# Kernel optimization log

Measured on AMD Instinct MI355X. Metric: run time of the kernel, lower is better.

## Reference

```python
import jax, jax.numpy as jnp
import numpy as np

B, K, N = 32768, 8, 64
TN = 3 * N


def _P():
    # 9x9 vec-transpose permutation (matches the hand-built P in the torch module)
    P = np.zeros((9, 9), dtype=np.float32)
    rows = [0, 1, 2, 3, 4, 5, 6, 7, 8]
    cols = [0, 3, 6, 1, 4, 7, 2, 5, 8]
    P[rows, cols] = 1.0
    return jnp.asarray(P)


def _precompute(b, w, lam):
    # b: (K,3,N), w: (1,N,1), lam: scalar
    wsum = jnp.sum(w)
    b_w = (b @ w)[..., 0] / wsum                       # (K,3)
    sw = jnp.sqrt(w).reshape(1, 1, N)                  # (1,1,N)
    bar_b = sw * (b - b_w[:, :, None])                 # (K,3,N)
    bar_B = bar_b.transpose(0, 2, 1).reshape(K, TN).T  # (3N,K)
    bar_H = 2.0 * (bar_B.T @ bar_B + lam * jnp.eye(K, dtype=b.dtype))
    Hinv = jnp.linalg.inv(bar_H)
    Htemp = Hinv @ jnp.ones((K, 1), dtype=b.dtype)     # (K,1)
    s = jnp.sum(Htemp)
    G = Hinv - (Htemp @ Htemp.T) / s                   # (K,K)
    g = Htemp / s                                      # (K,1)
    M = jnp.concatenate([
        2.0 * bar_B @ (G @ bar_B.T) - jnp.eye(TN, dtype=b.dtype),  # (3N,3N)
        2.0 * jnp.sqrt(lam) * (G @ bar_B.T),                        # (K,3N)
    ], axis=0)                                         # (3N+K,3N)
    h = jnp.concatenate([bar_B @ g, jnp.sqrt(lam) * g], axis=0)  # (3N+K,1)
    return bar_B, G, g, M, h, b_w, wsum


def setup_inputs() -> dict:
    key = jax.random.key(0)
    k1, k2 = jax.random.split(key)
    y = jax.random.normal(k1, (B, 3, N), dtype=jnp.float32)
    b = jax.random.normal(k2, (K, 3, N), dtype=jnp.float32)
    w = jnp.ones((1, N, 1), dtype=jnp.float32)
    lam = jnp.ones((1,), dtype=jnp.float32)
    return {"y": y, "b": b, "w": w, "lam": lam}


def reference(y, b, w, lam):
    lam = jnp.squeeze(lam)
    Pm = _P()
    bar_B, G, g, M, h, b_w, wsum = _precompute(b, w, lam)

    # weighted centroid + centered/weighted keypoints
    y_w = (y @ w) / wsum                               # (B,3,1)
    sw = jnp.sqrt(w).reshape(1, 1, N)
    bar_y = sw * (y - y_w)                             # (B,3,N)

    # Batched Q build. kron(Y^T, I3) contraction done implicitly:
    # (M @ kron(Y^T,I3))[a, 3m+j] = sum_n M[a,3n+j] * Y[m,n]
    M_r = M.reshape(TN + K, N, 3)                      # (A,N,3)
    E = jnp.einsum('anj,bmn->bamj', M_r, bar_y).reshape(B, TN + K, 9) @ Pm  # tempE: (B,A,9)
    q_top = jnp.einsum('a,bae->be', h[:, 0], E)        # Q[0,1:]: (B,9)
    Q00 = jnp.sum(h * h)
    Q_low = jnp.einsum('bae,baf->bef', E, E)           # Q[1:,1:]: (B,9,9)

    Q = jnp.zeros((B, 10, 10), dtype=y.dtype)
    Q = Q.at[:, 0, 0].set(Q00)
    Q = Q.at[:, 0, 1:].set(q_top)
    Q = Q.at[:, 1:, 0].set(q_top)
    Q = Q.at[:, 1:, 1:].set(Q_low)

    # Tight SDP relaxation solution: X* = v v^T with v the eigenvector of Q
    # at the smallest eigenvalue; the original then takes top eigvec of X,
    # which recovers the same v.
    ev, evec = jnp.linalg.eigh(Q)
    vec = evec[:, :, 0]                                # smallest-eigenvalue eigvec, (B,10)
    vec = vec / vec[:, :1]
    R = vec[:, 1:].reshape(B, 3, 3).transpose(0, 2, 1)  # (B,3,3)

    # shape coefficients: c = 2 * G bar_B^T kron(I_N, R^T) vec(bar_y^T) + g
    A = G @ bar_B.T                                    # (K,3N)
    Bv = jnp.einsum('bji,bjn->bni', R, bar_y).reshape(B, TN, 1)
    c = 2.0 * (A @ Bv) + g                             # (B,K,1)

    # translation
    t = y_w - R @ (b_w.T @ c)                          # (B,3,1)
    return R, t, c
```

## Files before the change

### kernel.cpp

```cpp
#include <hip/hip_runtime.h>
#include <math.h>

static constexpr int Bn = 32768;

__host__ __device__ constexpr int tidx(int i, int j) { return i*10 - i*(i+1)/2 + j; }
__host__ __device__ constexpr int lidx(int i, int j) { return i*(i+1)/2 + j; }

__global__ __launch_bounds__(256, 2) void k_main(const float* __restrict__ y,
                                                 const float* __restrict__ bb,
                                                 const float* __restrict__ w,
                                                 const float* __restrict__ lam,
                                                 float* __restrict__ out)
{
  __shared__ float s_w[64], s_sw[64], s_barb[64][25];
  __shared__ float s_BtB[64];
  __shared__ float s_M[8][16];
  __shared__ float s_u[8], s_red[64];
  __shared__ float s_wsum, s_q00;
  __shared__ float s_cb[4*520];
  __shared__ float s_G[64], s_g8[8], s_bw[24];
  __shared__ float s_Q[55][66];

  const int t   = threadIdx.x;
  const bool act = (t < 64);
  const int i8 = (t & 63) >> 3, j8 = t & 7;
  const float lv = lam[0];

  if (act) {
    s_w[t]  = w[t];
    s_sw[t] = sqrtf(fmaxf(w[t], 0.0f));
  }
  __syncthreads();
  if (t == 0) { float a = 0; for (int n = 0; n < 64; n++) a += s_w[n]; s_wsum = a; }
  __syncthreads();
  const float wsum = s_wsum;
  if (t < 24) {
    float a = 0;
    for (int n = 0; n < 64; n++) a += bb[t*64 + n] * s_w[n];
    s_bw[t] = a / wsum;
  }
  __syncthreads();
  if (act)
    for (int km = 0; km < 24; ++km)
      s_barb[t][km] = s_sw[t] * (bb[km*64 + t] - s_bw[km]);
  __syncthreads();
  if (act) {
    float a = 0;
    for (int n = 0; n < 64; n++)
      for (int j = 0; j < 3; j++)
        a += s_barb[n][i8*3 + j] * s_barb[n][j8*3 + j];
    s_BtB[t] = a;
  }
  __syncthreads();
  if (act) {
    s_M[i8][j8]     = 2.0f * (s_BtB[t] + ((i8 == j8) ? lv : 0.0f));
    s_M[i8][8 + j8] = (i8 == j8) ? 1.0f : 0.0f;
  }
#pragma unroll
  for (int k = 0; k < 8; k++) {
    __syncthreads();
    float fk = 0.0f, piv = 1.0f;
    if (act) { fk = s_M[i8][k]; piv = 1.0f / s_M[k][k]; }
    __syncthreads();
    if (act && i8 == k) { s_M[k][j8] *= piv; s_M[k][8 + j8] *= piv; }
    __syncthreads();
    if (act && i8 != k) {
      s_M[i8][j8]     -= fk * s_M[k][j8];
      s_M[i8][8 + j8] -= fk * s_M[k][8 + j8];
    }
  }
  __syncthreads();
  if (t < 8) {
    float a = 0;
#pragma unroll
    for (int j = 0; j < 8; j++) a += s_M[t][8 + j];
    s_u[t] = a;
  }
  __syncthreads();
  if (t == 0) {
    float s = 0;
#pragma unroll
    for (int j = 0; j < 8; j++) s += s_u[j];
    s_red[0] = s;
  }
  __syncthreads();
  {
    const float s = s_red[0];
    if (t < 8) s_g8[t] = s_u[t] / s;
    if (act) s_G[t] = s_M[i8][8 + j8] - s_u[i8] * s_u[j8] / s;
  }
  __syncthreads();
  if (act) s_red[t] = s_g8[i8] * (s_BtB[t] + ((i8 == j8) ? lv : 0.0f)) * s_g8[j8];
  __syncthreads();
  if (t == 0) {
    float a = 0;
    for (int n = 0; n < 64; n++) a += s_red[n];
    s_q00 = a;
  }
  if (act) {
    float* p = s_cb + (t >> 4)*520 + (t & 15)*32;
    p[0] = s_w[t]; p[1] = 0; p[2] = 0; p[3] = 0;
#pragma unroll
    for (int km = 0; km < 24; km++)
      p[4 + km] = s_sw[t] * s_barb[t][km];
#pragma unroll
    for (int i = 28; i < 32; i++) p[i] = 0;
  }
  __syncthreads();
  const float q00v = s_q00;

  const int lb  = t >> 2;
  const int sub = t & 3;
  const int b   = blockIdx.x * 64 + lb;
  const float* yb = y + (size_t)b * 192;
  float F[24][3];
  float gw[6];
  float ywa[3] = {0, 0, 0};
#pragma unroll
  for (int i = 0; i < 24; i++) { F[i][0] = 0; F[i][1] = 0; F[i][2] = 0; }
#pragma unroll
  for (int i = 0; i < 6; i++) gw[i] = 0;

  const float* plane = s_cb + sub*520;
#pragma unroll
  for (int i4 = 0; i4 < 4; i4++) {
    const int n4 = sub*4 + i4;
    float4 v0 = reinterpret_cast<const float4*>(yb)[n4];
    float4 v1 = reinterpret_cast<const float4*>(yb + 64)[n4];
    float4 v2 = reinterpret_cast<const float4*>(yb + 128)[n4];
    float a0[4] = {v0.x, v0.y, v0.z, v0.w};
    float a1[4] = {v1.x, v1.y, v1.z, v1.w};
    float a2[4] = {v2.x, v2.y, v2.z, v2.w};
#pragma unroll
    for (int l = 0; l < 4; l++) {
      const int ni = 4*i4 + l;
      const float4* row = reinterpret_cast<const float4*>(plane + ni*32);
      float4 c0 = row[0];
      float4 ch[6];
#pragma unroll
      for (int cc = 0; cc < 6; cc++) ch[cc] = row[1 + cc];
      const float cb[24] = {ch[0].x, ch[0].y, ch[0].z, ch[0].w,
                            ch[1].x, ch[1].y, ch[1].z, ch[1].w,
                            ch[2].x, ch[2].y, ch[2].z, ch[2].w,
                            ch[3].x, ch[3].y, ch[3].z, ch[3].w,
                            ch[4].x, ch[4].y, ch[4].z, ch[4].w,
                            ch[5].x, ch[5].y, ch[5].z, ch[5].w};
      float ym0 = a0[l], ym1 = a1[l], ym2 = a2[l];
      float wn  = c0.x;
      float wy0 = wn*ym0, wy1 = wn*ym1, wy2 = wn*ym2;
      ywa[0] += wy0; ywa[1] += wy1; ywa[2] += wy2;
      gw[0] += wy0*ym0; gw[1] += wy0*ym1; gw[2] += wy0*ym2;
      gw[3] += wy1*ym1; gw[4] += wy1*ym2; gw[5] += wy2*ym2;
#pragma unroll
      for (int km = 0; km < 24; km++) {
        F[km][0] += cb[km]*ym0; F[km][1] += cb[km]*ym1; F[km][2] += cb[km]*ym2;
      }
    }
  }
#pragma unroll
  for (int km = 0; km < 24; km++)
#pragma unroll
    for (int m = 0; m < 3; m++) {
      float v = F[km][m];
      v += __shfl_xor(v, 1);
      v += __shfl_xor(v, 2);
      F[km][m] = v;
    }
#pragma unroll
  for (int i = 0; i < 6; i++) { float v = gw[i]; v += __shfl_xor(v, 1); v += __shfl_xor(v, 2); gw[i] = v; }
#pragma unroll
  for (int i = 0; i < 3; i++) { float v = ywa[i]; v += __shfl_xor(v, 1); v += __shfl_xor(v, 2); ywa[i] = v; }

  const float iws = 1.0f / wsum;
  float yw[3] = {ywa[0]*iws, ywa[1]*iws, ywa[2]*iws};
  float Gram[6];
  Gram[0] = gw[0] - ywa[0]*ywa[0]*iws;
  Gram[1] = gw[1] - ywa[0]*ywa[1]*iws;
  Gram[2] = gw[2] - ywa[0]*ywa[2]*iws;
  Gram[3] = gw[3] - ywa[1]*ywa[1]*iws;
  Gram[4] = gw[4] - ywa[1]*ywa[2]*iws;
  Gram[5] = gw[5] - ywa[2]*ywa[2]*iws;

  if (sub == 0) s_Q[0][lb] = q00v;
#pragma unroll
  for (int e = 0; e < 9; e++) {
    const int j = e / 3, m = e % 3;
    float a = 0;
#pragma unroll
    for (int k = 0; k < 8; k++) a += s_g8[k] * F[k*3 + j][m];
    if ((e & 3) == sub) s_Q[tidx(0, 1 + e)][lb] = -a;
  }
  float F6[6][3];
#pragma unroll
  for (int kk = 0; kk < 6; kk++)
#pragma unroll
    for (int m = 0; m < 3; m++) {
      float x01 = (sub & 1) ? F[6 + kk][m]  : F[kk][m];
      float x23 = (sub & 1) ? F[18 + kk][m] : F[12 + kk][m];
      F6[kk][m] = (sub & 2) ? x23 : x01;
    }
  float FGr[2][9];
#pragma unroll
  for (int kk = 0; kk < 2; kk++) {
    float gcol[8];
#pragma unroll
    for (int k = 0; k < 8; k++) {
      float g01 = (sub & 1) ? s_G[k*8 + 2 + kk] : s_G[k*8 + 0 + kk];
      float g23 = (sub & 1) ? s_G[k*8 + 6 + kk] : s_G[k*8 + 4 + kk];
      gcol[k] = (sub & 2) ? g23 : g01;
    }
#pragma unroll
    for (int e = 0; e < 9; e++) {
      const int j = e / 3, m = e % 3;
      float a = 0;
#pragma unroll
      for (int k = 0; k < 8; k++) a += gcol[k] * F[k*3 + j][m];
      FGr[kk][e] = a;
    }
  }
#pragma unroll
  for (int e = 0; e < 9; e++)
#pragma unroll
    for (int f = e; f < 9; f++) {
      const int j = e/3, m = e%3, j2 = f/3, m2 = f%3;
      float p = FGr[0][e] * F6[j2][m2] + FGr[1][e] * F6[3 + j2][m2];
      p += __shfl_xor(p, 1);
      p += __shfl_xor(p, 2);
      if ((tidx(1 + e, 1 + f) & 3) == sub) {
        const float gterm = (j == j2) ? Gram[(m <= m2) ? (m*3 - m*(m+1)/2 + m2) : (m2*3 - m2*(m2+1)/2 + m)] : 0.0f;
        s_Q[tidx(1 + e, 1 + f)][lb] = -2.0f*p + gterm;
      }
    }
  __syncthreads();

  float Mm[55];
#pragma unroll
  for (int i = 0; i < 10; i++)
#pragma unroll
    for (int j = 0; j <= i; j++)
      Mm[lidx(i,j)] = s_Q[tidx(j,i)][lb];

  float tr = 0.0f, hi = Mm[lidx(0,0)];
#pragma unroll
  for (int j = 0; j < 10; j++) {
    tr += Mm[lidx(j,j)];
    hi = fminf(hi, Mm[lidx(j,j)]);
  }

  float ad[10], b2[9], bofd[9];
#pragma unroll
  for (int j = 0; j < 8; j++) {
    float s2 = 0;
#pragma unroll
    for (int i = j + 1; i < 10; i++) s2 += Mm[lidx(i,j)] * Mm[lidx(i,j)];
    const float x0 = Mm[lidx(j+1,j)];
    const float anorm = __builtin_amdgcn_sqrtf(s2);
    const float alpha = (x0 > 0.0f) ? -anorm : anorm;
    const float uu = s2 - alpha * x0;
    const float beta = (uu > 1e-35f) ? __builtin_amdgcn_rcpf(uu) : 0.0f;
    float u[10], p[10];
    u[j+1] = x0 - alpha;
#pragma unroll
    for (int i = j + 2; i < 10; i++) u[i] = Mm[lidx(i,j)];
#pragma unroll
    for (int i = j + 1; i < 10; i++) {
      float acc = 0;
#pragma unroll
      for (int k = j + 1; k < 10; k++) acc += Mm[(i >= k) ? lidx(i,k) : lidx(k,i)] * u[k];
      p[i] = beta * acc;
    }
    float K = 0;
#pragma unroll
    for (int i = j + 1; i < 10; i++) K += u[i] * p[i];
    K *= 0.5f * beta;
#pragma unroll
    for (int i = j + 1; i < 10; i++) p[i] -= K * u[i];
#pragma unroll
    for (int i = j + 1; i < 10; i++)
#pragma unroll
      for (int k = j + 1; k <= i; k++)
        Mm[lidx(i,k)] -= u[i]*p[k] + p[i]*u[k];
    ad[j]   = Mm[lidx(j,j)];
    b2[j]   = s2;
    bofd[j] = alpha;
  }
  ad[8] = Mm[lidx(8,8)];
  ad[9] = Mm[lidx(9,9)];
  bofd[8] = Mm[lidx(9,8)];
  b2[8] = bofd[8] * bofd[8];

  float b2max = b2[0];
#pragma unroll
  for (int i = 1; i < 9; i++) b2max = fmaxf(b2max, b2[i]);
  const float pm = 1e-20f * b2max + 1e-30f;

  float lo = 0.0f;
  const int base = (t & 63) & ~3;
  const float subf = (sub == 0) ? 2.0f : (float)sub;
  for (int round = 0; round < 11; ++round) {
    const float quart = 0.25f * (hi - lo);
    const float mid = lo + quart * subf;
    int neg = 0;
    float d = ad[0] - mid;
    neg += (d < 0.0f) ? 1 : 0;
#pragma unroll
    for (int i = 1; i < 10; i++) {
      d = (fabsf(d) < pm) ? -pm : d;
      d = ad[i] - mid - b2[i-1] * __builtin_amdgcn_rcpf(d);
      neg += (d < 0.0f) ? 1 : 0;
    }
    const int n1 = __shfl(neg, base | 1);
    const int n2 = __shfl(neg, base | 2);
    const int n3 = __shfl(neg, base | 3);
    const float m1 = lo + quart, m2v = lo + 2.0f*quart, m3 = lo + 3.0f*quart;
    const float nlo = (n3 == 0) ? m3 : (n2 == 0) ? m2v : (n1 == 0) ? m1 : lo;
    const float nhi = (n1 > 0) ? m1 : (n2 > 0) ? m2v : (n3 > 0) ? m3 : hi;
    lo = nlo; hi = nhi;
  }

  const float delta = 1e-5f * fabsf(tr) + 1e-30f;
  const float sigma = lo - delta;
  float dt[10], lt[9], idt[10];
  dt[0] = ad[0] - sigma;
#pragma unroll
  for (int i = 0; i < 9; i++) {
    float dd = fmaxf(dt[i], 1e-30f);
    float inv = __builtin_amdgcn_rcpf(dd);
    idt[i] = inv;
    lt[i] = bofd[i] * inv;
    dt[i+1] = ad[i+1] - sigma - lt[i]*bofd[i];
  }
  dt[9] = fmaxf(dt[9], 1e-30f);
  idt[9] = __builtin_amdgcn_rcpf(dt[9]);

  float z[10];
#pragma unroll
  for (int i = 0; i < 10; i++) z[i] = 1.0f;
#pragma unroll
  for (int it = 0; it < 3; ++it) {
#pragma unroll
    for (int i = 1; i < 10; i++) z[i] -= lt[i-1]*z[i-1];
#pragma unroll
    for (int i = 0; i < 10; i++) z[i] *= idt[i];
#pragma unroll
    for (int i = 8; i >= 0; i--) z[i] -= lt[i]*z[i+1];
    float s2 = 0;
#pragma unroll
    for (int i = 0; i < 10; i++) s2 += z[i]*z[i];
    float sc = __builtin_amdgcn_rsqf(s2 + 1e-38f);
#pragma unroll
    for (int i = 0; i < 10; i++) z[i] *= sc;
  }
#pragma unroll
  for (int j = 7; j >= 0; j--) {
    const float x0 = Mm[lidx(j+1,j)];
    const float us = x0 - bofd[j];
    const float uu = b2[j] - bofd[j]*x0;
    const float beta = (uu > 1e-35f) ? __builtin_amdgcn_rcpf(uu) : 0.0f;
    float dot = us * z[j+1];
#pragma unroll
    for (int i = j + 2; i < 10; i++) dot += Mm[lidx(i,j)] * z[i];
    const float f = beta * dot;
    z[j+1] -= f * us;
#pragma unroll
    for (int i = j + 2; i < 10; i++) z[i] -= f * Mm[lidx(i,j)];
  }

  const float inv0 = __builtin_amdgcn_rcpf(z[0]);
  float R[3][3];
#pragma unroll
  for (int r = 0; r < 3; r++)
#pragma unroll
    for (int cc = 0; cc < 3; cc++)
      R[r][cc] = z[1 + 3*cc + r] * inv0;

  float cv[2];
#pragma unroll
  for (int kk = 0; kk < 2; kk++) {
    const int k = sub*2 + kk;
    float a = 0;
#pragma unroll
    for (int e = 0; e < 9; e++) a += z[1 + e] * FGr[kk][e];
    cv[kk] = 2.0f * inv0 * a + s_g8[k];
    out[(size_t)12*Bn + (size_t)b*8 + k] = cv[kk];
  }
  float um0 = s_bw[(sub*2)*3 + 0]*cv[0] + s_bw[(sub*2 + 1)*3 + 0]*cv[1];
  float um1 = s_bw[(sub*2)*3 + 1]*cv[0] + s_bw[(sub*2 + 1)*3 + 1]*cv[1];
  float um2 = s_bw[(sub*2)*3 + 2]*cv[0] + s_bw[(sub*2 + 1)*3 + 2]*cv[1];
  um0 += __shfl_xor(um0, 1); um0 += __shfl_xor(um0, 2);
  um1 += __shfl_xor(um1, 1); um1 += __shfl_xor(um1, 2);
  um2 += __shfl_xor(um2, 1); um2 += __shfl_xor(um2, 2);

#pragma unroll
  for (int r = 0; r < 3; r++)
#pragma unroll
    for (int cc = 0; cc < 3; cc++)
      if (((r*3 + cc) & 3) == sub)
        out[(size_t)b*9 + r*3 + cc] = R[r][cc];
  if (sub == 0) {
#pragma unroll
    for (int r = 0; r < 3; r++)
      out[(size_t)9*Bn + (size_t)b*3 + r] = yw[r] - (R[r][0]*um0 + R[r][1]*um1 + R[r][2]*um2);
  }
}

extern "C" void kernel_launch(void* const* d_in, const int* in_sizes, int n_in,
                              void* d_out, int out_size, void* d_ws, size_t ws_size,
                              hipStream_t stream) {
  const float* y   = (const float*)d_in[0];
  const float* bb  = (const float*)d_in[1];
  const float* w   = (const float*)d_in[2];
  const float* lam = (const float*)d_in[3];
  float* out = (float*)d_out;
  (void)d_ws; (void)ws_size;
  k_main<<<Bn/64, 256, 0, stream>>>(y, bb, w, lam, out);
}
```

Measured before the change: 36.21 us.

## Prefetch y before precompute, merge Gauss-Jordan barriers, cut bisection rounds

Moves the per-batch y loads to the start of the kernel so their global-memory latency overlaps the per-block precompute phase (centroids, BtB, 8x8 inversion). The Gauss-Jordan elimination now reads the pivot row into registers and applies normalization and elimination in one step, dropping one barrier per pivot. The eigenvalue bisection runs 9 rounds instead of 11, which cuts arithmetic but lowers the precision of the smallest-eigenvalue estimate. Holding 48 extra floats of y in registers across the precompute raises register pressure under launch_bounds(256,2).

```diff
diff --git a/kernel.cpp b/kernel.cpp
--- a/kernel.cpp
+++ b/kernel.cpp
@@ -26,6 +26,19 @@
   const int i8 = (t & 63) >> 3, j8 = t & 7;
   const float lv = lam[0];
 
+  const int lb  = t >> 2;
+  const int sub = t & 3;
+  const int b   = blockIdx.x * 64 + lb;
+  const float* yb = y + (size_t)b * 192;
+  float4 vy0[4], vy1[4], vy2[4];
+#pragma unroll
+  for (int i4 = 0; i4 < 4; i4++) {
+    const int n4 = sub*4 + i4;
+    vy0[i4] = reinterpret_cast<const float4*>(yb)[n4];
+    vy1[i4] = reinterpret_cast<const float4*>(yb + 64)[n4];
+    vy2[i4] = reinterpret_cast<const float4*>(yb + 128)[n4];
+  }
+
   if (act) {
     s_w[t]  = w[t];
     s_sw[t] = sqrtf(fmaxf(w[t], 0.0f));
@@ -59,14 +72,22 @@
 #pragma unroll
   for (int k = 0; k < 8; k++) {
     __syncthreads();
-    float fk = 0.0f, piv = 1.0f;
-    if (act) { fk = s_M[i8][k]; piv = 1.0f / s_M[k][k]; }
+    float fk = 0.0f, pivv = 1.0f, rk0 = 0.0f, rk1 = 0.0f;
+    if (act) {
+      fk   = s_M[i8][k];
+      pivv = s_M[k][k];
+      rk0  = s_M[k][j8];
+      rk1  = s_M[k][8 + j8];
+    }
     __syncthreads();
-    if (act && i8 == k) { s_M[k][j8] *= piv; s_M[k][8 + j8] *= piv; }
-    __syncthreads();
-    if (act && i8 != k) {
-      s_M[i8][j8]     -= fk * s_M[k][j8];
-      s_M[i8][8 + j8] -= fk * s_M[k][8 + j8];
+    if (act) {
+      const float ip = 1.0f / pivv;
+      if (i8 == k) { s_M[k][j8] = rk0 * ip; s_M[k][8 + j8] = rk1 * ip; }
+      else {
+        const float f = fk * ip;
+        s_M[i8][j8]     -= f * rk0;
+        s_M[i8][8 + j8] -= f * rk1;
+      }
     }
   }
   __syncthreads();
@@ -109,10 +130,6 @@
   __syncthreads();
   const float q00v = s_q00;
 
-  const int lb  = t >> 2;
-  const int sub = t & 3;
-  const int b   = blockIdx.x * 64 + lb;
-  const float* yb = y + (size_t)b * 192;
   float F[24][3];
   float gw[6];
   float ywa[3] = {0, 0, 0};
@@ -124,13 +141,9 @@
   const float* plane = s_cb + sub*520;
 #pragma unroll
   for (int i4 = 0; i4 < 4; i4++) {
-    const int n4 = sub*4 + i4;
-    float4 v0 = reinterpret_cast<const float4*>(yb)[n4];
-    float4 v1 = reinterpret_cast<const float4*>(yb + 64)[n4];
-    float4 v2 = reinterpret_cast<const float4*>(yb + 128)[n4];
-    float a0[4] = {v0.x, v0.y, v0.z, v0.w};
-    float a1[4] = {v1.x, v1.y, v1.z, v1.w};
-    float a2[4] = {v2.x, v2.y, v2.z, v2.w};
+    float a0[4] = {vy0[i4].x, vy0[i4].y, vy0[i4].z, vy0[i4].w};
+    float a1[4] = {vy1[i4].x, vy1[i4].y, vy1[i4].z, vy1[i4].w};
+    float a2[4] = {vy2[i4].x, vy2[i4].y, vy2[i4].z, vy2[i4].w};
 #pragma unroll
     for (int l = 0; l < 4; l++) {
       const int ni = 4*i4 + l;
@@ -297,7 +310,7 @@
   float lo = 0.0f;
   const int base = (t & 63) & ~3;
   const float subf = (sub == 0) ? 2.0f : (float)sub;
-  for (int round = 0; round < 11; ++round) {
+  for (int round = 0; round < 9; ++round) {
     const float quart = 0.25f * (hi - lo);
     const float mid = lo + quart * subf;
     int neg = 0;
```

Result: slower. 37.66 us (+4.0%).
